# Kernel optimization log

Hardware: AMD Instinct MI355X
Metric: run time of the kernel (lower is better)

The kernel has to match this reference:

```python
import jax, jax.numpy as jnp
import numpy as np

TEMPERATURE = 0.1

def _l2norm(x):
    # F.normalize(dim=1) with eps clamp
    n = jnp.maximum(jnp.linalg.norm(x, axis=1, keepdims=True), 1e-12)
    return x / n

def _retrieval_metric(s):
    # T=1: position of the diagonal element in each row's descending sort.
    order = jnp.argsort(-s, axis=1)            # [N,N] descending argsort
    rankpos = jnp.argsort(order, axis=1)        # inverse permutation: rank of each column
    pos = jnp.diagonal(rankpos)                 # j such that rank[i][j] == i
    posf = pos.astype(s.dtype)
    r1 = jnp.mean((pos < 1).astype(s.dtype))
    r5 = jnp.mean((pos < 5).astype(s.dtype))
    r10 = jnp.mean((pos < 10).astype(s.dtype))
    mr = jnp.mean(posf)
    return r1, r5, r10, mr

def setup_inputs() -> dict:
    key = jax.random.key(0)
    k1, k2, k3, k4 = jax.random.split(key, 4)
    N, C = 4096, 512
    return {
        'v_feat': jax.random.normal(k1, (N, C), dtype=jnp.float32),
        't_feat': jax.random.normal(k2, (N, C), dtype=jnp.float32),
        'p_v': jax.random.normal(k3, (N, C), dtype=jnp.float32),
        'p_t': jax.random.normal(k4, (N, C), dtype=jnp.float32),
    }

def reference(v_feat, t_feat, p_v, p_t):
    vn = _l2norm(v_feat)
    tn = _l2norm(t_feat)
    pvn = _l2norm(p_v)
    ptn = _l2norm(p_t)
    sv = jnp.einsum('nc,mc->nm', vn, ptn) / TEMPERATURE  # [N,N]
    st = jnp.einsum('nc,mc->nm', tn, pvn) / TEMPERATURE  # [N,N]
    # nominator: scalar logsumexp over both diagonals (2N values)
    nominator = jax.nn.logsumexp(jnp.concatenate([jnp.diagonal(sv), jnp.diagonal(st)], axis=0))
    # denominator: per-row logsumexp over concatenated [N,2N]
    denominator = jax.nn.logsumexp(jnp.concatenate([sv, st], axis=1), axis=1)
    loss = jnp.mean(denominator - nominator)
    # metrics (no-grad path in original)
    v_std = jnp.mean(jnp.std(vn, axis=0, ddof=1))
    t_std = jnp.mean(jnp.std(tn, axis=0, ddof=1))
    pv_std = jnp.mean(jnp.std(pvn, axis=0, ddof=1))
    pt_std = jnp.mean(jnp.std(ptn, axis=0, ddof=1))
    sv_raw = jnp.einsum('nc,mc->nm', vn, ptn)
    st_raw = jnp.einsum('nc,mc->nm', tn, pvn)
    v_r1, v_r5, v_r10, v_mr = _retrieval_metric(sv_raw)
    t_r1, t_r5, t_r10, t_mr = _retrieval_metric(st_raw)
    return (loss, v_std, t_std, pv_std, pt_std,
            v_r1, v_r5, v_r10, v_mr,
            t_r1, t_r5, t_r10, t_mr)
```

## Files before the change

kernel.cpp:

```cpp
#include <hip/hip_runtime.h>
#include <hip/hip_bf16.h>

#define N 4096
#define C 512

typedef __attribute__((ext_vector_type(8))) short bf16x8;
typedef __attribute__((ext_vector_type(8))) short s16x8;
typedef __attribute__((ext_vector_type(4))) float f32x4;

__device__ inline float bf2f(__hip_bfloat16 h) { return __bfloat162float(h); }

__device__ inline void gload16(const void* g, void* l) {
    __builtin_amdgcn_global_load_lds(
        (__attribute__((address_space(1))) void*)(g),
        (__attribute__((address_space(3))) void*)(l),
        16, 0, 0);
}

__global__ __launch_bounds__(256) void k_prep(
    const float* __restrict__ s0, const float* __restrict__ s1f,
    const float* __restrict__ s2f, const float* __restrict__ s3,
    __hip_bfloat16* __restrict__ ws_hi0, long mat_stride,
    float* __restrict__ dv, float* __restrict__ dt,
    float* __restrict__ st1, float* __restrict__ st2,
    unsigned int* __restrict__ counter)
{
    __shared__ float sa[4][512];
    __shared__ float sq[4][512];

    const int b = blockIdx.x;
    const int tid = threadIdx.x;
    const int lane = tid & 63;
    const int w = tid >> 6;

    if (b == 0 && tid == 0) *counter = 0;

    const int m = b >> 8;
    const int chunk = b & 255;
    const float* src = (m == 0) ? s0 : (m == 1) ? s1f : (m == 2) ? s2f : s3;
    const float* srcB = (m == 0) ? s3 : s2f;
    float* dout = (m == 0) ? dv : dt;
    __hip_bfloat16* hi = ws_hi0 + (long)m * mat_stride;
    __hip_bfloat16* lo = hi + (long)N * C;

    float a[8], q[8];
    for (int e = 0; e < 8; e++) { a[e] = 0.f; q[e] = 0.f; }

    const int row0 = chunk * 16 + w * 4;
    for (int i = 0; i < 4; i++) {
        const int row = row0 + i;
        const float4* r4 = (const float4*)(src + (size_t)row * C);
        float4 x0 = r4[lane * 2];
        float4 x1 = r4[lane * 2 + 1];
        float ss = x0.x*x0.x + x0.y*x0.y + x0.z*x0.z + x0.w*x0.w
                 + x1.x*x1.x + x1.y*x1.y + x1.z*x1.z + x1.w*x1.w;
        for (int o = 1; o < 64; o <<= 1) ss += __shfl_xor(ss, o);
        float scale = 1.0f / fmaxf(sqrtf(ss), 1e-12f);

        float y[8] = { x0.x*scale, x0.y*scale, x0.z*scale, x0.w*scale,
                       x1.x*scale, x1.y*scale, x1.z*scale, x1.w*scale };
        __hip_bfloat16 hv[8], lv[8];
        for (int e = 0; e < 8; e++) {
            hv[e] = __float2bfloat16(y[e]);
            lv[e] = __float2bfloat16(y[e] - bf2f(hv[e]));
            a[e] += y[e];
            q[e] += y[e] * y[e];
        }
        size_t base = (size_t)row * C + lane * 8;
        *(s16x8*)(hi + base) = *(s16x8*)hv;
        *(s16x8*)(lo + base) = *(s16x8*)lv;

        if (m < 2) {
            const float4* b4 = (const float4*)(srcB + (size_t)row * C);
            float4 b0 = b4[lane * 2], b1 = b4[lane * 2 + 1];
            float ssb = b0.x*b0.x + b0.y*b0.y + b0.z*b0.z + b0.w*b0.w
                      + b1.x*b1.x + b1.y*b1.y + b1.z*b1.z + b1.w*b1.w;
            float dot = x0.x*b0.x + x0.y*b0.y + x0.z*b0.z + x0.w*b0.w
                      + x1.x*b1.x + x1.y*b1.y + x1.z*b1.z + x1.w*b1.w;
            for (int o = 1; o < 64; o <<= 1) {
                ssb += __shfl_xor(ssb, o);
                dot += __shfl_xor(dot, o);
            }
            if (lane == 0)
                dout[row] = dot * scale / fmaxf(sqrtf(ssb), 1e-12f);
        }
    }

    for (int e = 0; e < 8; e++) {
        sa[w][lane * 8 + e] = a[e];
        sq[w][lane * 8 + e] = q[e];
    }
    __syncthreads();
    for (int c = tid; c < 512; c += 256) {
        float A = sa[0][c] + sa[1][c] + sa[2][c] + sa[3][c];
        float B = sq[0][c] + sq[1][c] + sq[2][c] + sq[3][c];
        size_t o = ((size_t)m * 256 + chunk) * 512 + c;
        st1[o] = A;
        st2[o] = B;
    }
}

__global__ __launch_bounds__(256) void k_gemm(
    const __hip_bfloat16* __restrict__ h0, const __hip_bfloat16* __restrict__ l0,
    const __hip_bfloat16* __restrict__ h1, const __hip_bfloat16* __restrict__ l1,
    const __hip_bfloat16* __restrict__ h2, const __hip_bfloat16* __restrict__ l2,
    const __hip_bfloat16* __restrict__ h3, const __hip_bfloat16* __restrict__ l3,
    const float* __restrict__ dv, const float* __restrict__ dt,
    float* __restrict__ pev, float* __restrict__ pet,
    float* __restrict__ pcv, float* __restrict__ pct)
{
    __shared__ __align__(16) __hip_bfloat16 sA[2][128][32];
    __shared__ __align__(16) __hip_bfloat16 sB[2][128][32];
    __shared__ float sdiag[128];
    __shared__ float sred[128][2][2];

    const int z = blockIdx.z;
    const __hip_bfloat16* Ah = z ? h1 : h0;
    const __hip_bfloat16* Al = z ? l1 : l0;
    const __hip_bfloat16* Bh = z ? h2 : h3;
    const __hip_bfloat16* Bl = z ? l2 : l3;
    const float* diag = z ? dt : dv;
    float* pe = z ? pet : pev;
    float* pc = z ? pct : pcv;

    const int tid = threadIdx.x;
    const int lane = tid & 63;
    const int w = tid >> 6;
    const int wy = w >> 1, wx = w & 1;
    const int bm = blockIdx.x * 128;
    const int bn = blockIdx.y * 128;

    if (tid < 128) sdiag[tid] = diag[bm + tid];

    f32x4 acc[4][4];
    for (int i = 0; i < 4; i++)
        for (int j = 0; j < 4; j++)
            acc[i][j] = (f32x4){0.f, 0.f, 0.f, 0.f};

    const int srow = lane >> 2;
    const int lcol = (lane & 3) * 8;
    const int scolg = (((lane & 3) ^ ((lane >> 3) & 3))) * 8;
    const int fr = lane & 15;
    const int pcs = ((lane >> 4) ^ ((fr >> 1) & 3)) * 8;

    for (int k0 = 0; k0 < C; k0 += 32) {
        for (int half = 0; half < 2; half++) {
            int rr = w * 16 + half * 64 + srow;
            size_t ga = (size_t)(bm + rr) * C + k0 + scolg;
            size_t gb = (size_t)(bn + rr) * C + k0 + scolg;
            gload16(Ah + ga, &sA[0][rr][lcol]);
            gload16(Al + ga, &sA[1][rr][lcol]);
            gload16(Bh + gb, &sB[0][rr][lcol]);
            gload16(Bl + gb, &sB[1][rr][lcol]);
        }
        __syncthreads();

        bf16x8 a_h[4], a_l[4], b_h[4], b_l[4];
        for (int i = 0; i < 4; i++) {
            a_h[i] = *(const bf16x8*)&sA[0][wy * 64 + i * 16 + fr][pcs];
            a_l[i] = *(const bf16x8*)&sA[1][wy * 64 + i * 16 + fr][pcs];
            b_h[i] = *(const bf16x8*)&sB[0][wx * 64 + i * 16 + fr][pcs];
            b_l[i] = *(const bf16x8*)&sB[1][wx * 64 + i * 16 + fr][pcs];
        }
        for (int i = 0; i < 4; i++)
            for (int j = 0; j < 4; j++) {
                acc[i][j] = __builtin_amdgcn_mfma_f32_16x16x32_bf16(a_h[i], b_h[j], acc[i][j], 0, 0, 0);
                acc[i][j] = __builtin_amdgcn_mfma_f32_16x16x32_bf16(a_h[i], b_l[j], acc[i][j], 0, 0, 0);
                acc[i][j] = __builtin_amdgcn_mfma_f32_16x16x32_bf16(a_l[i], b_h[j], acc[i][j], 0, 0, 0);
            }
        __syncthreads();
    }

    const int quad = lane >> 4;
    for (int i = 0; i < 4; i++) {
        for (int reg = 0; reg < 4; reg++) {
            int rloc = wy * 64 + i * 16 + quad * 4 + reg;
            int grow = bm + rloc;
            float d = sdiag[rloc];
            float e = 0.f, c = 0.f;
            for (int j = 0; j < 4; j++) {
                float s = acc[i][j][reg];
                int gcol = bn + wx * 64 + j * 16 + fr;
                e += __expf(10.f * s - 10.f);
                if (s > d && gcol != grow) c += 1.f;
            }
            for (int o = 1; o < 16; o <<= 1) {
                e += __shfl_xor(e, o);
                c += __shfl_xor(c, o);
            }
            if (fr == 0) { sred[rloc][wx][0] = e; sred[rloc][wx][1] = c; }
        }
    }
    __syncthreads();
    if (tid < 128) {
        size_t idx = (size_t)(bm + tid) * 32 + blockIdx.y;
        pe[idx] = sred[tid][0][0] + sred[tid][1][0];
        pc[idx] = sred[tid][0][1] + sred[tid][1][1];
    }
}

__global__ __launch_bounds__(64) void k_fin(
    const float* __restrict__ dv, const float* __restrict__ dt,
    const float* __restrict__ pev, const float* __restrict__ pet,
    const float* __restrict__ pcv, const float* __restrict__ pct,
    const float* __restrict__ st1, const float* __restrict__ st2,
    float* __restrict__ partials, float* __restrict__ stdpart,
    unsigned int* __restrict__ counter, float* __restrict__ out)
{
    const int b = blockIdx.x;
    const int lane = threadIdx.x;

    if (b < 64) {
        const int row = b * 64 + lane;
        float se = 0.f, pv = 0.f, pt = 0.f;
        const float4* e4v = (const float4*)(pev + (size_t)row * 32);
        const float4* e4t = (const float4*)(pet + (size_t)row * 32);
        const float4* c4v = (const float4*)(pcv + (size_t)row * 32);
        const float4* c4t = (const float4*)(pct + (size_t)row * 32);
        for (int qd = 0; qd < 8; qd++) {
            float4 aa = e4v[qd], bb = e4t[qd], cc = c4v[qd], dd = c4t[qd];
            se += aa.x + aa.y + aa.z + aa.w + bb.x + bb.y + bb.z + bb.w;
            pv += cc.x + cc.y + cc.z + cc.w;
            pt += dd.x + dd.y + dd.z + dd.w;
        }
        float vals[10];
        vals[0] = logf(se) + 10.f;
        vals[1] = (pv < 0.5f) ? 1.f : 0.f;
        vals[2] = (pv < 4.5f) ? 1.f : 0.f;
        vals[3] = (pv < 9.5f) ? 1.f : 0.f;
        vals[4] = pv;
        vals[5] = (pt < 0.5f) ? 1.f : 0.f;
        vals[6] = (pt < 4.5f) ? 1.f : 0.f;
        vals[7] = (pt < 9.5f) ? 1.f : 0.f;
        vals[8] = pt;
        vals[9] = __expf(10.f * dv[row] - 10.f) + __expf(10.f * dt[row] - 10.f);
        for (int k = 0; k < 10; k++) {
            float v = vals[k];
            for (int o = 1; o < 64; o <<= 1) v += __shfl_xor(v, o);
            if (lane == k) partials[(size_t)b * 10 + k] = v;
        }
    } else {
        const int idx = b - 64;
        const int m = idx >> 3;
        const int col = (idx & 7) * 64 + lane;
        float a = 0.f, q = 0.f;
        for (int ch = 0; ch < 256; ch++) {
            size_t o = ((size_t)m * 256 + ch) * 512 + col;
            a += st1[o];
            q += st2[o];
        }
        float var = (q - a * a * (1.f / N)) * (1.f / (N - 1));
        float sd = sqrtf(fmaxf(var, 0.f));
        for (int o = 1; o < 64; o <<= 1) sd += __shfl_xor(sd, o);
        if (lane == 0) stdpart[idx] = sd;
    }

    __syncthreads();
    __shared__ unsigned int s_old;
    if (lane == 0) {
        __threadfence();
        s_old = atomicAdd(counter, 1u);
    }
    __syncthreads();
    if (s_old != 95) return;
    __threadfence();

    float v = 0.f;
    if (lane < 10) {
        for (int k = 0; k < 64; k++) v += partials[k * 10 + lane];
    }
    __shared__ float g[10];
    __shared__ float stds[4];
    if (lane < 10) g[lane] = v;
    if (lane < 4) {
        float s = 0.f;
        for (int i = 0; i < 8; i++) s += stdpart[lane * 8 + i];
        stds[lane] = s * (1.f / 512.f);
    }
    __syncthreads();
    if (lane == 0) {
        const float invN = 1.f / N;
        float nominator = logf(g[9]) + 10.f;
        out[0]  = g[0] * invN - nominator;
        out[1]  = stds[0];
        out[2]  = stds[1];
        out[3]  = stds[2];
        out[4]  = stds[3];
        out[5]  = g[1] * invN;
        out[6]  = g[2] * invN;
        out[7]  = g[3] * invN;
        out[8]  = g[4] * invN;
        out[9]  = g[5] * invN;
        out[10] = g[6] * invN;
        out[11] = g[7] * invN;
        out[12] = g[8] * invN;
    }
}

extern "C" void kernel_launch(void* const* d_in, const int* in_sizes, int n_in,
                              void* d_out, int out_size, void* d_ws, size_t ws_size,
                              hipStream_t stream)
{
    char* p = (char*)d_ws;
    const size_t NE = (size_t)N * C;
    const long mat_stride = 2 * NE;
    __hip_bfloat16* hiA[4];
    __hip_bfloat16* loA[4];
    for (int m = 0; m < 4; m++) {
        hiA[m] = (__hip_bfloat16*)p; p += NE * 2;
        loA[m] = (__hip_bfloat16*)p; p += NE * 2;
    }
    float* dv  = (float*)p; p += N * 4;
    float* dt  = (float*)p; p += N * 4;
    float* pev = (float*)p; p += 32 * N * 4;
    float* pet = (float*)p; p += 32 * N * 4;
    float* pcv = (float*)p; p += 32 * N * 4;
    float* pct = (float*)p; p += 32 * N * 4;
    float* st1 = (float*)p; p += 4 * 256 * 512 * 4;
    float* st2 = (float*)p; p += 4 * 256 * 512 * 4;
    float* partials = (float*)p; p += 64 * 10 * 4;
    float* stdpart  = (float*)p; p += 32 * 4;
    unsigned int* counter = (unsigned int*)p; p += 16;

    k_prep<<<dim3(1024), 256, 0, stream>>>(
        (const float*)d_in[0], (const float*)d_in[1],
        (const float*)d_in[2], (const float*)d_in[3],
        hiA[0], mat_stride, dv, dt, st1, st2, counter);

    k_gemm<<<dim3(32, 32, 2), 256, 0, stream>>>(
        hiA[0], loA[0], hiA[1], loA[1], hiA[2], loA[2], hiA[3], loA[3],
        dv, dt, pev, pet, pcv, pct);

    k_fin<<<dim3(96), 64, 0, stream>>>(
        dv, dt, pev, pet, pcv, pct, st1, st2,
        partials, stdpart, counter, (float*)d_out);
}
```

Before: 214.0 us.

## Replace partial-sum buffers with atomic accumulators and pair-wise prep loads

The prep kernel now processes each paired input (X and its partner B) in one block, so the partner rows read for the diagonal dot product are also normalized and stored instead of being loaded a second time. Column statistics and per-row exp/count partials are accumulated with global atomics into small zeroed buffers instead of large per-chunk and per-tile arrays. The finisher becomes a single block with no counter handshake. This cuts workspace traffic and reduction work at the cost of an extra memset launch, atomic contention, and non-deterministic float summation order.

```diff
diff --git a/kernel.cpp b/kernel.cpp
--- a/kernel.cpp
+++ b/kernel.cpp
@@ -22,8 +22,7 @@
     const float* __restrict__ s2f, const float* __restrict__ s3,
     __hip_bfloat16* __restrict__ ws_hi0, long mat_stride,
     float* __restrict__ dv, float* __restrict__ dt,
-    float* __restrict__ st1, float* __restrict__ st2,
-    unsigned int* __restrict__ counter)
+    float* __restrict__ colsum, float* __restrict__ colsq)
 {
     __shared__ float sa[4][512];
     __shared__ float sq[4][512];
@@ -33,70 +32,76 @@
     const int lane = tid & 63;
     const int w = tid >> 6;
 
-    if (b == 0 && tid == 0) *counter = 0;
-
-    const int m = b >> 8;
+    const int pair = b >> 8;
     const int chunk = b & 255;
-    const float* src = (m == 0) ? s0 : (m == 1) ? s1f : (m == 2) ? s2f : s3;
-    const float* srcB = (m == 0) ? s3 : s2f;
-    float* dout = (m == 0) ? dv : dt;
-    __hip_bfloat16* hi = ws_hi0 + (long)m * mat_stride;
-    __hip_bfloat16* lo = hi + (long)N * C;
-
-    float a[8], q[8];
-    for (int e = 0; e < 8; e++) { a[e] = 0.f; q[e] = 0.f; }
+    const float* X = pair ? s1f : s0;
+    const float* B = pair ? s2f : s3;
+    const int mX = pair ? 1 : 0;
+    const int mB = pair ? 2 : 3;
+    __hip_bfloat16* hiX = ws_hi0 + (long)mX * mat_stride;
+    __hip_bfloat16* loX = hiX + (long)N * C;
+    __hip_bfloat16* hiB = ws_hi0 + (long)mB * mat_stride;
+    __hip_bfloat16* loB = hiB + (long)N * C;
+    float* dout = pair ? dt : dv;
+
+    float aX[8], qX[8], aB[8], qB[8];
+    for (int e = 0; e < 8; e++) { aX[e] = 0.f; qX[e] = 0.f; aB[e] = 0.f; qB[e] = 0.f; }
 
     const int row0 = chunk * 16 + w * 4;
     for (int i = 0; i < 4; i++) {
         const int row = row0 + i;
-        const float4* r4 = (const float4*)(src + (size_t)row * C);
-        float4 x0 = r4[lane * 2];
-        float4 x1 = r4[lane * 2 + 1];
-        float ss = x0.x*x0.x + x0.y*x0.y + x0.z*x0.z + x0.w*x0.w
-                 + x1.x*x1.x + x1.y*x1.y + x1.z*x1.z + x1.w*x1.w;
-        for (int o = 1; o < 64; o <<= 1) ss += __shfl_xor(ss, o);
-        float scale = 1.0f / fmaxf(sqrtf(ss), 1e-12f);
-
-        float y[8] = { x0.x*scale, x0.y*scale, x0.z*scale, x0.w*scale,
-                       x1.x*scale, x1.y*scale, x1.z*scale, x1.w*scale };
-        __hip_bfloat16 hv[8], lv[8];
+        const float4* x4 = (const float4*)(X + (size_t)row * C);
+        const float4* b4 = (const float4*)(B + (size_t)row * C);
+        float4 x0 = x4[lane * 2], x1 = x4[lane * 2 + 1];
+        float4 b0 = b4[lane * 2], b1 = b4[lane * 2 + 1];
+
+        float ss  = x0.x*x0.x + x0.y*x0.y + x0.z*x0.z + x0.w*x0.w
+                  + x1.x*x1.x + x1.y*x1.y + x1.z*x1.z + x1.w*x1.w;
+        float ssb = b0.x*b0.x + b0.y*b0.y + b0.z*b0.z + b0.w*b0.w
+                  + b1.x*b1.x + b1.y*b1.y + b1.z*b1.z + b1.w*b1.w;
+        float dot = x0.x*b0.x + x0.y*b0.y + x0.z*b0.z + x0.w*b0.w
+                  + x1.x*b1.x + x1.y*b1.y + x1.z*b1.z + x1.w*b1.w;
+        for (int o = 1; o < 64; o <<= 1) {
+            ss  += __shfl_xor(ss, o);
+            ssb += __shfl_xor(ssb, o);
+            dot += __shfl_xor(dot, o);
+        }
+        float scX = 1.0f / fmaxf(sqrtf(ss), 1e-12f);
+        float scB = 1.0f / fmaxf(sqrtf(ssb), 1e-12f);
+        if (lane == 0) dout[row] = dot * scX * scB;
+
+        float yx[8] = { x0.x*scX, x0.y*scX, x0.z*scX, x0.w*scX,
+                        x1.x*scX, x1.y*scX, x1.z*scX, x1.w*scX };
+        float yb[8] = { b0.x*scB, b0.y*scB, b0.z*scB, b0.w*scB,
+                        b1.x*scB, b1.y*scB, b1.z*scB, b1.w*scB };
+        __hip_bfloat16 hvx[8], lvx[8], hvb[8], lvb[8];
         for (int e = 0; e < 8; e++) {
-            hv[e] = __float2bfloat16(y[e]);
-            lv[e] = __float2bfloat16(y[e] - bf2f(hv[e]));
-            a[e] += y[e];
-            q[e] += y[e] * y[e];
+            hvx[e] = __float2bfloat16(yx[e]);
+            lvx[e] = __float2bfloat16(yx[e] - bf2f(hvx[e]));
+            aX[e] += yx[e]; qX[e] += yx[e] * yx[e];
+            hvb[e] = __float2bfloat16(yb[e]);
+            lvb[e] = __float2bfloat16(yb[e] - bf2f(hvb[e]));
+            aB[e] += yb[e]; qB[e] += yb[e] * yb[e];
         }
         size_t base = (size_t)row * C + lane * 8;
-        *(s16x8*)(hi + base) = *(s16x8*)hv;
-        *(s16x8*)(lo + base) = *(s16x8*)lv;
-
-        if (m < 2) {
-            const float4* b4 = (const float4*)(srcB + (size_t)row * C);
-            float4 b0 = b4[lane * 2], b1 = b4[lane * 2 + 1];
-            float ssb = b0.x*b0.x + b0.y*b0.y + b0.z*b0.z + b0.w*b0.w
-                      + b1.x*b1.x + b1.y*b1.y + b1.z*b1.z + b1.w*b1.w;
-            float dot = x0.x*b0.x + x0.y*b0.y + x0.z*b0.z + x0.w*b0.w
-                      + x1.x*b1.x + x1.y*b1.y + x1.z*b1.z + x1.w*b1.w;
-            for (int o = 1; o < 64; o <<= 1) {
-                ssb += __shfl_xor(ssb, o);
-                dot += __shfl_xor(dot, o);
-            }
-            if (lane == 0)
-                dout[row] = dot * scale / fmaxf(sqrtf(ssb), 1e-12f);
-        }
-    }
-
-    for (int e = 0; e < 8; e++) {
-        sa[w][lane * 8 + e] = a[e];
-        sq[w][lane * 8 + e] = q[e];
-    }
+        *(s16x8*)(hiX + base) = *(s16x8*)hvx;
+        *(s16x8*)(loX + base) = *(s16x8*)lvx;
+        *(s16x8*)(hiB + base) = *(s16x8*)hvb;
+        *(s16x8*)(loB + base) = *(s16x8*)lvb;
+    }
+
+    for (int e = 0; e < 8; e++) { sa[w][lane*8+e] = aX[e]; sq[w][lane*8+e] = qX[e]; }
     __syncthreads();
     for (int c = tid; c < 512; c += 256) {
-        float A = sa[0][c] + sa[1][c] + sa[2][c] + sa[3][c];
-        float B = sq[0][c] + sq[1][c] + sq[2][c] + sq[3][c];
-        size_t o = ((size_t)m * 256 + chunk) * 512 + c;
-        st1[o] = A;
-        st2[o] = B;
+        atomicAdd(&colsum[mX * 512 + c], sa[0][c] + sa[1][c] + sa[2][c] + sa[3][c]);
+        atomicAdd(&colsq [mX * 512 + c], sq[0][c] + sq[1][c] + sq[2][c] + sq[3][c]);
+    }
+    __syncthreads();
+    for (int e = 0; e < 8; e++) { sa[w][lane*8+e] = aB[e]; sq[w][lane*8+e] = qB[e]; }
+    __syncthreads();
+    for (int c = tid; c < 512; c += 256) {
+        atomicAdd(&colsum[mB * 512 + c], sa[0][c] + sa[1][c] + sa[2][c] + sa[3][c]);
+        atomicAdd(&colsq [mB * 512 + c], sq[0][c] + sq[1][c] + sq[2][c] + sq[3][c]);
     }
 }
 
@@ -106,8 +111,8 @@
     const __hip_bfloat16* __restrict__ h2, const __hip_bfloat16* __restrict__ l2,
     const __hip_bfloat16* __restrict__ h3, const __hip_bfloat16* __restrict__ l3,
     const float* __restrict__ dv, const float* __restrict__ dt,
-    float* __restrict__ pev, float* __restrict__ pet,
-    float* __restrict__ pcv, float* __restrict__ pct)
+    float* __restrict__ row_ev, float* __restrict__ row_et,
+    float* __restrict__ row_cv, float* __restrict__ row_ct)
 {
     __shared__ __align__(16) __hip_bfloat16 sA[2][128][32];
     __shared__ __align__(16) __hip_bfloat16 sB[2][128][32];
@@ -120,8 +125,8 @@
     const __hip_bfloat16* Bh = z ? h2 : h3;
     const __hip_bfloat16* Bl = z ? l2 : l3;
     const float* diag = z ? dt : dv;
-    float* pe = z ? pet : pev;
-    float* pc = z ? pct : pcv;
+    float* row_e = z ? row_et : row_ev;
+    float* row_c = z ? row_ct : row_cv;
 
     const int tid = threadIdx.x;
     const int lane = tid & 63;
@@ -193,92 +198,68 @@
     }
     __syncthreads();
     if (tid < 128) {
-        size_t idx = (size_t)(bm + tid) * 32 + blockIdx.y;
-        pe[idx] = sred[tid][0][0] + sred[tid][1][0];
-        pc[idx] = sred[tid][0][1] + sred[tid][1][1];
-    }
-}
-
-__global__ __launch_bounds__(64) void k_fin(
+        atomicAdd(&row_e[bm + tid], sred[tid][0][0] + sred[tid][1][0]);
+        atomicAdd(&row_c[bm + tid], sred[tid][0][1] + sred[tid][1][1]);
+    }
+}
+
+__global__ __launch_bounds__(256) void k_fin(
     const float* __restrict__ dv, const float* __restrict__ dt,
-    const float* __restrict__ pev, const float* __restrict__ pet,
-    const float* __restrict__ pcv, const float* __restrict__ pct,
-    const float* __restrict__ st1, const float* __restrict__ st2,
-    float* __restrict__ partials, float* __restrict__ stdpart,
-    unsigned int* __restrict__ counter, float* __restrict__ out)
+    const float* __restrict__ row_ev, const float* __restrict__ row_et,
+    const float* __restrict__ row_cv, const float* __restrict__ row_ct,
+    const float* __restrict__ colsum, const float* __restrict__ colsq,
+    float* __restrict__ out)
 {
-    const int b = blockIdx.x;
-    const int lane = threadIdx.x;
-
-    if (b < 64) {
-        const int row = b * 64 + lane;
-        float se = 0.f, pv = 0.f, pt = 0.f;
-        const float4* e4v = (const float4*)(pev + (size_t)row * 32);
-        const float4* e4t = (const float4*)(pet + (size_t)row * 32);
-        const float4* c4v = (const float4*)(pcv + (size_t)row * 32);
-        const float4* c4t = (const float4*)(pct + (size_t)row * 32);
-        for (int qd = 0; qd < 8; qd++) {
-            float4 aa = e4v[qd], bb = e4t[qd], cc = c4v[qd], dd = c4t[qd];
-            se += aa.x + aa.y + aa.z + aa.w + bb.x + bb.y + bb.z + bb.w;
-            pv += cc.x + cc.y + cc.z + cc.w;
-            pt += dd.x + dd.y + dd.z + dd.w;
-        }
-        float vals[10];
-        vals[0] = logf(se) + 10.f;
-        vals[1] = (pv < 0.5f) ? 1.f : 0.f;
-        vals[2] = (pv < 4.5f) ? 1.f : 0.f;
-        vals[3] = (pv < 9.5f) ? 1.f : 0.f;
-        vals[4] = pv;
-        vals[5] = (pt < 0.5f) ? 1.f : 0.f;
-        vals[6] = (pt < 4.5f) ? 1.f : 0.f;
-        vals[7] = (pt < 9.5f) ? 1.f : 0.f;
-        vals[8] = pt;
-        vals[9] = __expf(10.f * dv[row] - 10.f) + __expf(10.f * dt[row] - 10.f);
-        for (int k = 0; k < 10; k++) {
-            float v = vals[k];
-            for (int o = 1; o < 64; o <<= 1) v += __shfl_xor(v, o);
-            if (lane == k) partials[(size_t)b * 10 + k] = v;
-        }
-    } else {
-        const int idx = b - 64;
-        const int m = idx >> 3;
-        const int col = (idx & 7) * 64 + lane;
-        float a = 0.f, q = 0.f;
-        for (int ch = 0; ch < 256; ch++) {
-            size_t o = ((size_t)m * 256 + ch) * 512 + col;
-            a += st1[o];
-            q += st2[o];
-        }
-        float var = (q - a * a * (1.f / N)) * (1.f / (N - 1));
-        float sd = sqrtf(fmaxf(var, 0.f));
-        for (int o = 1; o < 64; o <<= 1) sd += __shfl_xor(sd, o);
-        if (lane == 0) stdpart[idx] = sd;
-    }
-
-    __syncthreads();
-    __shared__ unsigned int s_old;
-    if (lane == 0) {
-        __threadfence();
-        s_old = atomicAdd(counter, 1u);
-    }
-    __syncthreads();
-    if (s_old != 95) return;
-    __threadfence();
-
-    float v = 0.f;
-    if (lane < 10) {
-        for (int k = 0; k < 64; k++) v += partials[k * 10 + lane];
-    }
-    __shared__ float g[10];
-    __shared__ float stds[4];
-    if (lane < 10) g[lane] = v;
-    if (lane < 4) {
-        float s = 0.f;
-        for (int i = 0; i < 8; i++) s += stdpart[lane * 8 + i];
-        stds[lane] = s * (1.f / 512.f);
-    }
-    __syncthreads();
-    if (lane == 0) {
+    const int t = threadIdx.x;
+    const int lane = t & 63;
+    const int wv = t >> 6;
+
+    float vals[10];
+    for (int k = 0; k < 10; k++) vals[k] = 0.f;
+    for (int i = 0; i < 16; i++) {
+        const int row = i * 256 + t;
+        float se = row_ev[row] + row_et[row];
+        float pv = row_cv[row];
+        float pt = row_ct[row];
+        vals[0] += logf(se) + 10.f;
+        vals[1] += (pv < 0.5f) ? 1.f : 0.f;
+        vals[2] += (pv < 4.5f) ? 1.f : 0.f;
+        vals[3] += (pv < 9.5f) ? 1.f : 0.f;
+        vals[4] += pv;
+        vals[5] += (pt < 0.5f) ? 1.f : 0.f;
+        vals[6] += (pt < 4.5f) ? 1.f : 0.f;
+        vals[7] += (pt < 9.5f) ? 1.f : 0.f;
+        vals[8] += pt;
+        vals[9] += __expf(10.f * dv[row] - 10.f) + __expf(10.f * dt[row] - 10.f);
+    }
+    __shared__ float red[4][10];
+    for (int k = 0; k < 10; k++) {
+        float v = vals[k];
+        for (int o = 1; o < 64; o <<= 1) v += __shfl_xor(v, o);
+        if (lane == 0) red[wv][k] = v;
+    }
+
+    __shared__ float smat[4][4];
+    for (int m = 0; m < 4; m++) {
+        float sd2 = 0.f;
+        for (int h = 0; h < 2; h++) {
+            int c = h * 256 + t;
+            float a = colsum[m * 512 + c];
+            float q = colsq [m * 512 + c];
+            float var = (q - a * a * (1.f / N)) * (1.f / (N - 1));
+            sd2 += sqrtf(fmaxf(var, 0.f));
+        }
+        for (int o = 1; o < 64; o <<= 1) sd2 += __shfl_xor(sd2, o);
+        if (lane == 0) smat[wv][m] = sd2;
+    }
+    __syncthreads();
+    if (t == 0) {
+        float g[10];
+        for (int k = 0; k < 10; k++)
+            g[k] = red[0][k] + red[1][k] + red[2][k] + red[3][k];
+        float stds[4];
+        for (int m = 0; m < 4; m++)
+            stds[m] = (smat[0][m] + smat[1][m] + smat[2][m] + smat[3][m]) * (1.f / 512.f);
         const float invN = 1.f / N;
         float nominator = logf(g[9]) + 10.f;
         out[0]  = g[0] * invN - nominator;
@@ -302,6 +283,15 @@
                               hipStream_t stream)
 {
     char* p = (char*)d_ws;
+
+    float* row_ev = (float*)p; p += N * 4;
+    float* row_et = (float*)p; p += N * 4;
+    float* row_cv = (float*)p; p += N * 4;
+    float* row_ct = (float*)p; p += N * 4;
+    float* colsum = (float*)p; p += 4 * 512 * 4;
+    float* colsq  = (float*)p; p += 4 * 512 * 4;
+    const size_t acc_bytes = (size_t)(p - (char*)d_ws);
+
     const size_t NE = (size_t)N * C;
     const long mat_stride = 2 * NE;
     __hip_bfloat16* hiA[4];
@@ -310,28 +300,20 @@
         hiA[m] = (__hip_bfloat16*)p; p += NE * 2;
         loA[m] = (__hip_bfloat16*)p; p += NE * 2;
     }
-    float* dv  = (float*)p; p += N * 4;
-    float* dt  = (float*)p; p += N * 4;
-    float* pev = (float*)p; p += 32 * N * 4;
-    float* pet = (float*)p; p += 32 * N * 4;
-    float* pcv = (float*)p; p += 32 * N * 4;
-    float* pct = (float*)p; p += 32 * N * 4;
-    float* st1 = (float*)p; p += 4 * 256 * 512 * 4;
-    float* st2 = (float*)p; p += 4 * 256 * 512 * 4;
-    float* partials = (float*)p; p += 64 * 10 * 4;
-    float* stdpart  = (float*)p; p += 32 * 4;
-    unsigned int* counter = (unsigned int*)p; p += 16;
-
-    k_prep<<<dim3(1024), 256, 0, stream>>>(
+    float* dv = (float*)p; p += N * 4;
+    float* dt = (float*)p; p += N * 4;
+
+    hipMemsetAsync(d_ws, 0, acc_bytes, stream);
+
+    k_prep<<<dim3(512), 256, 0, stream>>>(
         (const float*)d_in[0], (const float*)d_in[1],
         (const float*)d_in[2], (const float*)d_in[3],
-        hiA[0], mat_stride, dv, dt, st1, st2, counter);
+        hiA[0], mat_stride, dv, dt, colsum, colsq);
 
     k_gemm<<<dim3(32, 32, 2), 256, 0, stream>>>(
         hiA[0], loA[0], hiA[1], loA[1], hiA[2], loA[2], hiA[3], loA[3],
-        dv, dt, pev, pet, pcv, pct);
-
-    k_fin<<<dim3(96), 64, 0, stream>>>(
-        dv, dt, pev, pet, pcv, pct, st1, st2,
-        partials, stdpart, counter, (float*)d_out);
-}
+        dv, dt, row_ev, row_et, row_cv, row_ct);
+
+    k_fin<<<dim3(1), 256, 0, stream>>>(
+        dv, dt, row_ev, row_et, row_cv, row_ct, colsum, colsq, (float*)d_out);
+}
```

After: 212.2 us, median of 2. No clear change (-0.9%).
